# Kernel optimization log

Measured on AMD Instinct MI355X. Metric: run time of the kernel, lower is better.

Reference implementation:

```python
import jax, jax.numpy as jnp
import numpy as np

NUM_CLASSES = 8192
FEAT_DIM = 256
BATCH = 1024
TEMPERATURE = 0.1
BASE_TEMPERATURE = 0.1
PROTO_M = 0.5
EPS = 1e-12  # F.normalize eps


def setup_inputs() -> dict:
    key = jax.random.key(0)
    k1, k2, k3 = jax.random.split(key, 3)
    features = jax.random.normal(k1, (BATCH, FEAT_DIM), dtype=jnp.float32)
    proto = jax.random.normal(k2, (NUM_CLASSES, FEAT_DIM), dtype=jnp.float32)
    # prototypes buffer is unit-normalized after init_class_prototypes
    proto = proto / jnp.maximum(jnp.linalg.norm(proto, axis=1, keepdims=True), EPS)
    labels = jax.random.randint(k3, (BATCH,), 0, NUM_CLASSES, dtype=jnp.int64)
    return {"features": features, "prototypes": proto, "labels": labels}


def _forward(features, prototypes, labels):
    # Sequential per-sample EMA prototype update (order matters for repeated labels)
    def step(proto, fc):
        f, c = fc
        row = proto[c] * PROTO_M + f * (1.0 - PROTO_M)
        row = row / jnp.maximum(jnp.linalg.norm(row), EPS)
        return proto.at[c].set(row), None

    proto, _ = jax.lax.scan(step, prototypes, (features, labels))

    # Pairwise prototype similarity, masked (off-diagonal) mean of exp, then log
    logits = jnp.matmul(proto, proto.T) / TEMPERATURE          # [C, C]
    C = proto.shape[0]
    mask = 1.0 - jnp.eye(C, dtype=logits.dtype)                # zero diagonal
    neg_sum = jnp.sum(mask * jnp.exp(logits), axis=1)          # [C]
    mean_prob_neg = jnp.log(neg_sum / jnp.sum(mask, axis=1))
    # torch drops NaN rows before mean; nanmean reproduces that
    loss = (TEMPERATURE / BASE_TEMPERATURE) * jnp.nanmean(mean_prob_neg)
    return loss


def reference(features, prototypes, labels):
    return _forward(features, prototypes, labels)
```

## Files before the change

### kernel.cpp

```cpp
#include <hip/hip_runtime.h>
#include <hip/hip_bf16.h>
#include <math.h>

#define NUM_CLASSES 8192
#define FEAT_DIM    256
#define BATCH       1024

typedef long fp8x8;
typedef __attribute__((ext_vector_type(4))) float f32x4;

#define GLD16(gp, lp) __builtin_amdgcn_global_load_lds(                       \
    (const __attribute__((address_space(1))) void*)(gp),                      \
    (__attribute__((address_space(3))) void*)(lp), 16, 0, 0)

__global__ __launch_bounds__(256) void ema_convert_kernel(
    const float* __restrict__ feats, const float* __restrict__ proto,
    const int* __restrict__ labels, unsigned char* __restrict__ P8,
    float* __restrict__ rowsum) {
  __shared__ int lab_s[BATCH];
  const int tid = threadIdx.x;

  ((int4*)lab_s)[tid] = ((const int4*)labels)[tid];
  if (blockIdx.x < 32) rowsum[blockIdx.x * 256 + tid] = 0.0f;
  __syncthreads();

  const int c    = (blockIdx.x << 2) + (tid >> 6);
  const int lane = tid & 63;

  float4 p = ((const float4*)(proto + (size_t)c * FEAT_DIM))[lane];

  const int4 L0 = ((const int4*)lab_s)[lane * 4 + 0];
  const int4 L1 = ((const int4*)lab_s)[lane * 4 + 1];
  const int4 L2 = ((const int4*)lab_s)[lane * 4 + 2];
  const int4 L3 = ((const int4*)lab_s)[lane * 4 + 3];
  unsigned m = 0;
  m |= (L0.x == c) << 0;  m |= (L0.y == c) << 1;
  m |= (L0.z == c) << 2;  m |= (L0.w == c) << 3;
  m |= (L1.x == c) << 4;  m |= (L1.y == c) << 5;
  m |= (L1.z == c) << 6;  m |= (L1.w == c) << 7;
  m |= (L2.x == c) << 8;  m |= (L2.y == c) << 9;
  m |= (L2.z == c) << 10; m |= (L2.w == c) << 11;
  m |= (L3.x == c) << 12; m |= (L3.y == c) << 13;
  m |= (L3.z == c) << 14; m |= (L3.w == c) << 15;

  unsigned long long wm = __ballot(m != 0);
  while (wm) {
    const int src = __ffsll((long long)wm) - 1;
    unsigned mm = __shfl(m, src);
    while (mm) {
      const int j = __ffs(mm) - 1;
      mm &= mm - 1;
      const int t = src * 16 + j;
      float4 f = ((const float4*)(feats + (size_t)t * FEAT_DIM))[lane];
      float4 r;
      r.x = 0.5f * p.x + 0.5f * f.x;
      r.y = 0.5f * p.y + 0.5f * f.y;
      r.z = 0.5f * p.z + 0.5f * f.z;
      r.w = 0.5f * p.w + 0.5f * f.w;
      float ss = r.x * r.x + r.y * r.y + r.z * r.z + r.w * r.w;
#pragma unroll
      for (int off = 32; off; off >>= 1) ss += __shfl_xor(ss, off);
      float inv = 1.0f / fmaxf(sqrtf(ss), 1e-12f);
      p.x = r.x * inv; p.y = r.y * inv; p.z = r.z * inv; p.w = r.w * inv;
    }
    wm &= wm - 1;
  }

  int v = __builtin_amdgcn_cvt_pk_fp8_f32(p.x, p.y, 0, false);
  v = __builtin_amdgcn_cvt_pk_fp8_f32(p.z, p.w, v, true);
  ((int*)(P8 + (size_t)c * FEAT_DIM))[lane] = v;
}

#define NCHAIN 544

__global__ __launch_bounds__(256, 3) void gemm_rowsum_kernel(
    const unsigned char* __restrict__ P8, float* __restrict__ rowsum) {
  __shared__ __align__(16) char As[128 * 256];
  __shared__ __align__(16) char Bs[2][64 * 128];
  __shared__ float Lrow[2][128];
  __shared__ float Lcol[8][64];

  const int hw  = blockIdx.x;
  const int bid = (hw & 7) * (NCHAIN / 8) + (hw >> 3);

  int I = 0, rem = bid;
  while (rem >= ((64 - I + 3) >> 2)) { rem -= (64 - I + 3) >> 2; ++I; }
  const int Jstart = 2 * I + rem * 8;
  const int Lc = min(8, 128 - 2 * I - rem * 8);

  const int tid  = threadIdx.x;
  const int wid  = tid >> 6;
  const int lane = tid & 63;
  const int wm   = wid >> 1;
  const int wn   = wid & 1;
  const int g    = lane >> 4;
  const int rl   = lane & 15;

  ((float*)Lrow)[tid] = 0.0f;
  ((float*)Lcol)[tid] = 0.0f;
  ((float*)Lcol)[tid + 256] = 0.0f;

  {
    const unsigned char* PA = P8 + (size_t)(I * 128) * FEAT_DIM;
    const int rloc = lane >> 4;
    const int cph  = lane & 15;
#pragma unroll
    for (int q = 0; q < 8; ++q) {
      const int Ld = wid * 8 + q;
      const int r  = Ld * 4 + rloc;
      const int cs = cph ^ (r & 15);
      GLD16(PA + (size_t)r * FEAT_DIM + cs * 16, As + Ld * 1024);
    }
  }

  const int brloc = lane >> 3;
  const int bcph  = lane & 7;
#define SB(T, KT, BUF)                                                        \
  {                                                                           \
    const unsigned char* PB = P8 + (size_t)((Jstart + (T)) * 64) * FEAT_DIM;  \
    _Pragma("unroll")                                                         \
    for (int q = 0; q < 2; ++q) {                                             \
      const int Ld = wid * 2 + q;                                   \
      const int r  = Ld * 8 + brloc;                               \
      const int cs = bcph ^ (r & 7);                                          \
      GLD16(PB + (size_t)r * FEAT_DIM + (KT) * 128 + cs * 16,                 \
            Bs[BUF] + Ld * 1024);                                             \
    }                                                                         \
  }

  SB(0, 0, 0);
  __syncthreads();

  f32x4 acc[4][2] = {};

#define COMPUTE(KT, BUF)                                                      \
  {                                                                           \
    _Pragma("unroll")                                                         \
    for (int kk = 0; kk < 4; ++kk) {                                          \
      const int ca = ((KT) * 4 + kk) * 2 + (g >> 1);       \
      const int cb = kk * 2 + (g >> 1);                    \
      const int ib = (g & 1) * 8;                                             \
      fp8x8 a[4], b[2];                                                       \
      _Pragma("unroll")                                                       \
      for (int mi = 0; mi < 4; ++mi) {                                        \
        const int row = wm * 64 + mi * 16 + rl;                               \
        a[mi] = *(const fp8x8*)(As + row * 256 +                              \
                                ((ca ^ (row & 15)) << 4) + ib);               \
      }                                                                       \
      _Pragma("unroll")                                                       \
      for (int ni = 0; ni < 2; ++ni) {                                        \
        const int row = wn * 32 + ni * 16 + rl;                               \
        b[ni] = *(const fp8x8*)(Bs[BUF] + row * 128 +                         \
                                ((cb ^ (row & 7)) << 4) + ib);                \
      }                                                                       \
      _Pragma("unroll")                                                       \
      for (int mi = 0; mi < 4; ++mi)                                          \
        _Pragma("unroll")                                                     \
        for (int ni = 0; ni < 2; ++ni)                                        \
          acc[mi][ni] = __builtin_amdgcn_mfma_f32_16x16x32_fp8_fp8(           \
              a[mi], b[ni], acc[mi][ni], 0, 0, 0);                            \
    }                                                                         \
  }

#define EPI(T)                                                                \
  {                                                                           \
    const int Jt = Jstart + (T);                                              \
    const bool edge = ((Jt >> 1) == I);                                       \
    float col[2] = {0.0f, 0.0f};                                              \
    _Pragma("unroll")                                                         \
    for (int mi = 0; mi < 4; ++mi) {                                          \
      _Pragma("unroll")                                                       \
      for (int v = 0; v < 4; ++v) {                                           \
        const int lrow = wm * 64 + mi * 16 + g * 4 + v;                       \
        const int grow = I * 128 + lrow;                                      \
        float rs = 0.0f;                                                      \
        _Pragma("unroll")                                                     \
        for (int ni = 0; ni < 2; ++ni) {                                      \
          const int gcol = Jt * 64 + wn * 32 + ni * 16 + rl;                  \
          float e = __expf(10.0f * acc[mi][ni][v]);                           \
          if (edge && grow == gcol) e = 0.0f;                                 \
          rs += e;                                                            \
          col[ni] += e;                                                       \
        }                                                                     \
        rs += __shfl_xor(rs, 1);                                              \
        rs += __shfl_xor(rs, 2);                                              \
        rs += __shfl_xor(rs, 4);                                              \
        rs += __shfl_xor(rs, 8);                                              \
        if (rl == 0) Lrow[wn][lrow] += rs;         \
      }                                                                       \
    }                                                                         \
    _Pragma("unroll")                                                         \
    for (int ni = 0; ni < 2; ++ni) {                                          \
      float cs = col[ni];                                                     \
      cs += __shfl_xor(cs, 16);                                               \
      cs += __shfl_xor(cs, 32);                                               \
      if (g == 0)                                                             \
        atomicAdd(&Lcol[T][wn * 32 + ni * 16 + rl], cs);        \
    }                                                                         \
  }

  for (int t = 0; t < Lc; ++t) {
    SB(t, 1, 1);
    COMPUTE(0, 0);
    __syncthreads();
    if (t + 1 < Lc) SB(t + 1, 0, 0);
    COMPUTE(1, 1);
    EPI(t);
#pragma unroll
    for (int mi = 0; mi < 4; ++mi)
#pragma unroll
      for (int ni = 0; ni < 2; ++ni)
        acc[mi][ni] = (f32x4){0.0f, 0.0f, 0.0f, 0.0f};
    __syncthreads();
  }

  if (tid < 128)
    atomicAdd(&rowsum[I * 128 + tid], Lrow[0][tid] + Lrow[1][tid]);
  for (int idx = tid; idx < Lc * 64; idx += 256) {
    const int t = idx >> 6, c = idx & 63;
    const int Jt = Jstart + t;
    if ((Jt >> 1) != I)
      atomicAdd(&rowsum[Jt * 64 + c], Lcol[t][c]);
  }
}

__global__ __launch_bounds__(256) void finalize_kernel(
    const float* __restrict__ rowsum, float* __restrict__ out) {
  const int tid = threadIdx.x;
  float s = 0.0f;
  for (int i = tid; i < NUM_CLASSES; i += 256) {
    s += logf(rowsum[i] * (1.0f / (float)(NUM_CLASSES - 1)));
  }
#pragma unroll
  for (int off = 32; off; off >>= 1) s += __shfl_xor(s, off);
  __shared__ float red[4];
  if ((tid & 63) == 0) red[tid >> 6] = s;
  __syncthreads();
  if (tid == 0)
    out[0] = (red[0] + red[1] + red[2] + red[3]) * (1.0f / (float)NUM_CLASSES);
}

extern "C" void kernel_launch(void* const* d_in, const int* in_sizes, int n_in,
                              void* d_out, int out_size, void* d_ws, size_t ws_size,
                              hipStream_t stream) {
  const float* feats  = (const float*)d_in[0];
  const float* proto  = (const float*)d_in[1];
  const int*   labels = (const int*)d_in[2];
  float*       out    = (float*)d_out;

  char* ws = (char*)d_ws;
  unsigned char* P8 = (unsigned char*)ws;
  float* rowsum = (float*)(ws + (size_t)NUM_CLASSES * FEAT_DIM);

  ema_convert_kernel<<<NUM_CLASSES / 4, 256, 0, stream>>>(feats, proto, labels,
                                                          P8, rowsum);
  gemm_rowsum_kernel<<<NCHAIN, 256, 0, stream>>>(P8, rowsum);
  finalize_kernel<<<1, 256, 0, stream>>>(rowsum, out);
}
```

Baseline: 71.15 us.

## Hold A tile in registers and stream full-K 128-wide B tiles

Restructures the symmetric fp8 GEMM tile. Each wave now keeps its 32 rows of A for the whole K in registers, and the block loads full-K 128x128 B tiles into double-buffered LDS, replacing the 64-wide B tiles that were split in halves along K. Column partial sums go through per-wave LDS slots and a reduction instead of shared-memory atomics, and exp uses exp2f with a folded constant. The aim is fewer LDS reads of A and fewer barriers per tile. In exchange, register pressure and LDS use rise and occupancy drops from 3 to 2 blocks.

```diff
diff --git a/kernel.cpp b/kernel.cpp
--- a/kernel.cpp
+++ b/kernel.cpp
@@ -73,154 +73,139 @@
 
 #define NCHAIN 544
 
-__global__ __launch_bounds__(256, 3) void gemm_rowsum_kernel(
+__global__ __launch_bounds__(256, 2) void gemm_rowsum_kernel(
     const unsigned char* __restrict__ P8, float* __restrict__ rowsum) {
-  __shared__ __align__(16) char As[128 * 256];
-  __shared__ __align__(16) char Bs[2][64 * 128];
-  __shared__ float Lrow[2][128];
-  __shared__ float Lcol[8][64];
+  __shared__ __align__(16) char Bs[2][128 * 256];
+  __shared__ float Lrow[128];
+  __shared__ float Lcolw[4][128];
+  __shared__ float Lcolacc[4][128];
 
   const int hw  = blockIdx.x;
   const int bid = (hw & 7) * (NCHAIN / 8) + (hw >> 3);
 
   int I = 0, rem = bid;
   while (rem >= ((64 - I + 3) >> 2)) { rem -= (64 - I + 3) >> 2; ++I; }
-  const int Jstart = 2 * I + rem * 8;
-  const int Lc = min(8, 128 - 2 * I - rem * 8);
+  const int Jstart = I + rem * 4;
+  const int Lc = min(4, 64 - Jstart);
 
   const int tid  = threadIdx.x;
   const int wid  = tid >> 6;
   const int lane = tid & 63;
-  const int wm   = wid >> 1;
-  const int wn   = wid & 1;
   const int g    = lane >> 4;
   const int rl   = lane & 15;
 
-  ((float*)Lrow)[tid] = 0.0f;
-  ((float*)Lcol)[tid] = 0.0f;
-  ((float*)Lcol)[tid + 256] = 0.0f;
-
+  if (tid < 128) Lrow[tid] = 0.0f;
+
+  fp8x8 areg[2][8];
   {
-    const unsigned char* PA = P8 + (size_t)(I * 128) * FEAT_DIM;
-    const int rloc = lane >> 4;
-    const int cph  = lane & 15;
-#pragma unroll
-    for (int q = 0; q < 8; ++q) {
-      const int Ld = wid * 8 + q;
-      const int r  = Ld * 4 + rloc;
-      const int cs = cph ^ (r & 15);
-      GLD16(PA + (size_t)r * FEAT_DIM + cs * 16, As + Ld * 1024);
-    }
-  }
-
-  const int brloc = lane >> 3;
-  const int bcph  = lane & 7;
-#define SB(T, KT, BUF)                                                        \
+    const unsigned char* PA = P8 + (size_t)(I * 128 + wid * 32) * FEAT_DIM;
+#pragma unroll
+    for (int mi = 0; mi < 2; ++mi)
+#pragma unroll
+      for (int ks = 0; ks < 8; ++ks)
+        areg[mi][ks] = *(const fp8x8*)(PA + (mi * 16 + rl) * FEAT_DIM +
+                                       ks * 32 + g * 8);
+  }
+
+  const int brloc = lane >> 4;
+  const int bcph  = lane & 15;
+#define SB(JT, BUF)                                                           \
   {                                                                           \
-    const unsigned char* PB = P8 + (size_t)((Jstart + (T)) * 64) * FEAT_DIM;  \
-    _Pragma("unroll")                                                         \
-    for (int q = 0; q < 2; ++q) {                                             \
-      const int Ld = wid * 2 + q;                                   \
-      const int r  = Ld * 8 + brloc;                               \
-      const int cs = bcph ^ (r & 7);                                          \
-      GLD16(PB + (size_t)r * FEAT_DIM + (KT) * 128 + cs * 16,                 \
-            Bs[BUF] + Ld * 1024);                                             \
-    }                                                                         \
-  }
-
-  SB(0, 0, 0);
-  __syncthreads();
-
-  f32x4 acc[4][2] = {};
-
-#define COMPUTE(KT, BUF)                                                      \
+    const unsigned char* PB_ = P8 + (size_t)((JT) * 128) * FEAT_DIM;          \
+    _Pragma("unroll")                                                         \
+    for (int q = 0; q < 8; ++q) {                                             \
+      const int Ld = wid * 8 + q;                                  \
+      const int r  = Ld * 4 + brloc;                     \
+      const int cs = bcph ^ (r & 15);          \
+      GLD16(PB_ + (size_t)r * FEAT_DIM + cs * 16, &Bs[BUF][Ld * 1024]);       \
+    }                                                                         \
+  }
+
+  f32x4 acc[2][8] = {};
+
+#define COMPUTE(BUF)                                                          \
   {                                                                           \
-    _Pragma("unroll")                                                         \
-    for (int kk = 0; kk < 4; ++kk) {                                          \
-      const int ca = ((KT) * 4 + kk) * 2 + (g >> 1);       \
-      const int cb = kk * 2 + (g >> 1);                    \
-      const int ib = (g & 1) * 8;                                             \
-      fp8x8 a[4], b[2];                                                       \
+    const char* B_ = &Bs[BUF][0];                                             \
+    _Pragma("unroll")                                                         \
+    for (int ks = 0; ks < 8; ++ks) {                                          \
+      fp8x8 b[8];                                                             \
       _Pragma("unroll")                                                       \
-      for (int mi = 0; mi < 4; ++mi) {                                        \
-        const int row = wm * 64 + mi * 16 + rl;                               \
-        a[mi] = *(const fp8x8*)(As + row * 256 +                              \
-                                ((ca ^ (row & 15)) << 4) + ib);               \
+      for (int ni = 0; ni < 8; ++ni) {                                        \
+        const int row = ni * 16 + rl;                                         \
+        const int cl  = ks * 2 + (g >> 1);                                    \
+        b[ni] = *(const fp8x8*)(B_ + row * 256 +                              \
+                                ((cl ^ (row & 15)) << 4) + (g & 1) * 8);      \
       }                                                                       \
       _Pragma("unroll")                                                       \
-      for (int ni = 0; ni < 2; ++ni) {                                        \
-        const int row = wn * 32 + ni * 16 + rl;                               \
-        b[ni] = *(const fp8x8*)(Bs[BUF] + row * 128 +                         \
-                                ((cb ^ (row & 7)) << 4) + ib);                \
-      }                                                                       \
-      _Pragma("unroll")                                                       \
-      for (int mi = 0; mi < 4; ++mi)                                          \
+      for (int mi = 0; mi < 2; ++mi)                                          \
         _Pragma("unroll")                                                     \
-        for (int ni = 0; ni < 2; ++ni)                                        \
+        for (int ni = 0; ni < 8; ++ni)                                        \
           acc[mi][ni] = __builtin_amdgcn_mfma_f32_16x16x32_fp8_fp8(           \
-              a[mi], b[ni], acc[mi][ni], 0, 0, 0);                            \
+              areg[mi][ks], b[ni], acc[mi][ni], 0, 0, 0);                     \
     }                                                                         \
   }
 
 #define EPI(T)                                                                \
   {                                                                           \
-    const int Jt = Jstart + (T);                                              \
-    const bool edge = ((Jt >> 1) == I);                                       \
-    float col[2] = {0.0f, 0.0f};                                              \
-    _Pragma("unroll")                                                         \
-    for (int mi = 0; mi < 4; ++mi) {                                          \
+    const int  Jt    = Jstart + (T);                                          \
+    const bool diagb = (Jt == I);                                             \
+    float colp[8] = {0, 0, 0, 0, 0, 0, 0, 0};                                 \
+    _Pragma("unroll")                                                         \
+    for (int mi = 0; mi < 2; ++mi) {                                          \
       _Pragma("unroll")                                                       \
       for (int v = 0; v < 4; ++v) {                                           \
-        const int lrow = wm * 64 + mi * 16 + g * 4 + v;                       \
-        const int grow = I * 128 + lrow;                                      \
+        const int rstrip = wid * 32 + mi * 16 + g * 4 + v;                    \
         float rs = 0.0f;                                                      \
         _Pragma("unroll")                                                     \
-        for (int ni = 0; ni < 2; ++ni) {                                      \
-          const int gcol = Jt * 64 + wn * 32 + ni * 16 + rl;                  \
-          float e = __expf(10.0f * acc[mi][ni][v]);                           \
-          if (edge && grow == gcol) e = 0.0f;                                 \
+        for (int ni = 0; ni < 8; ++ni) {                                      \
+          float e = exp2f(14.4269504089f * acc[mi][ni][v]);                   \
+          if (diagb && rstrip == ni * 16 + rl) e = 0.0f;                      \
           rs += e;                                                            \
-          col[ni] += e;                                                       \
+          colp[ni] += e;                                                      \
         }                                                                     \
         rs += __shfl_xor(rs, 1);                                              \
         rs += __shfl_xor(rs, 2);                                              \
         rs += __shfl_xor(rs, 4);                                              \
         rs += __shfl_xor(rs, 8);                                              \
-        if (rl == 0) Lrow[wn][lrow] += rs;         \
+        if (rl == 0) Lrow[rstrip] += rs;                                      \
       }                                                                       \
     }                                                                         \
     _Pragma("unroll")                                                         \
-    for (int ni = 0; ni < 2; ++ni) {                                          \
-      float cs = col[ni];                                                     \
+    for (int ni = 0; ni < 8; ++ni) {                                          \
+      float cs = colp[ni];                                                    \
       cs += __shfl_xor(cs, 16);                                               \
       cs += __shfl_xor(cs, 32);                                               \
-      if (g == 0)                                                             \
-        atomicAdd(&Lcol[T][wn * 32 + ni * 16 + rl], cs);        \
-    }                                                                         \
-  }
-
+      if (g == 0) Lcolw[wid][ni * 16 + rl] = cs;                              \
+    }                                                                         \
+  }
+
+  SB(Jstart, 0);
+  __syncthreads();
+
+  int buf = 0;
   for (int t = 0; t < Lc; ++t) {
-    SB(t, 1, 1);
-    COMPUTE(0, 0);
-    __syncthreads();
-    if (t + 1 < Lc) SB(t + 1, 0, 0);
-    COMPUTE(1, 1);
+    if (t + 1 < Lc) SB(Jstart + t + 1, buf ^ 1);
+    COMPUTE(buf);
     EPI(t);
 #pragma unroll
-    for (int mi = 0; mi < 4; ++mi)
-#pragma unroll
-      for (int ni = 0; ni < 2; ++ni)
+    for (int mi = 0; mi < 2; ++mi)
+#pragma unroll
+      for (int ni = 0; ni < 8; ++ni)
         acc[mi][ni] = (f32x4){0.0f, 0.0f, 0.0f, 0.0f};
     __syncthreads();
-  }
-
-  if (tid < 128)
-    atomicAdd(&rowsum[I * 128 + tid], Lrow[0][tid] + Lrow[1][tid]);
-  for (int idx = tid; idx < Lc * 64; idx += 256) {
-    const int t = idx >> 6, c = idx & 63;
+    if (tid < 128)
+      Lcolacc[t][tid] = Lcolw[0][tid] + Lcolw[1][tid] +
+                        Lcolw[2][tid] + Lcolw[3][tid];
+    __syncthreads();
+    buf ^= 1;
+  }
+
+  if (tid < 128) atomicAdd(&rowsum[I * 128 + tid], Lrow[tid]);
+  for (int idx = tid; idx < Lc * 128; idx += 256) {
+    const int t = idx >> 7, c = idx & 127;
     const int Jt = Jstart + t;
-    if ((Jt >> 1) != I)
-      atomicAdd(&rowsum[Jt * 64 + c], Lcol[t][c]);
+    if (Jt != I)
+      atomicAdd(&rowsum[Jt * 128 + c], Lcolacc[t][c]);
   }
 }
 
```

Result: faster. 69.70 us (-2.0%).
